# Kernel tuning notes

Hardware: AMD Instinct MI355X
Metric: run time of the kernel (lower is better)

Reference implementation:

```python
import jax, jax.numpy as jnp
import numpy as np

B, HI, WI, CV, CT, T = 8, 64, 64, 512, 512, 77
HH, DH = 8, 64
TOP_M, TOPP, CLAMP_LOGIT, TAU, ALPHA0 = 5, 0.9, 2.0, 0.5, 0.1


def setup_inputs() -> dict:
    key = jax.random.key(0)
    ks = jax.random.split(key, 12)
    s = 0.02
    w = lambda k, shp: jax.random.normal(k, shp, jnp.float32) * s
    return {
        "visual": jax.random.normal(ks[0], (B, HI, WI, CV), jnp.float32),
        "text": jax.random.normal(ks[1], (B, T, CT), jnp.float32),
        "ln1_g": jnp.ones((CV,), jnp.float32), "ln1_b": jnp.zeros((CV,), jnp.float32),
        "ln2_g": jnp.ones((CV,), jnp.float32), "ln2_b": jnp.zeros((CV,), jnp.float32),
        "Wq": w(ks[2], (CV, CV)), "bq": jnp.zeros((CV,), jnp.float32),
        "Wk": w(ks[3], (CT, CV)), "bk": jnp.zeros((CV,), jnp.float32),
        "Wv": w(ks[4], (CT, CV)), "bv": jnp.zeros((CV,), jnp.float32),
        "Wo": w(ks[5], (CV, CV)), "bo": jnp.zeros((CV,), jnp.float32),
        "Wg": w(ks[6], (CV, 1)), "bg": jnp.zeros((1,), jnp.float32),
        "W1": w(ks[7], (CV, 4 * CV)), "b1": jnp.zeros((4 * CV,), jnp.float32),
        "W2": w(ks[8], (4 * CV, CV)), "b2": jnp.zeros((CV,), jnp.float32),
        "logit_scale": jnp.asarray(np.log(1.0 / 0.07), jnp.float32),
        "alpha": jnp.asarray(ALPHA0, jnp.float32),
    }


def _ln(x, g, b, eps=1e-5):
    m = x.mean(-1, keepdims=True)
    v = ((x - m) ** 2).mean(-1, keepdims=True)
    return (x - m) * jax.lax.rsqrt(v + eps) * g + b


def _l2norm(t, eps=1e-6):  # F.normalize: x / max(||x||, eps)
    return t / jnp.maximum(jnp.linalg.norm(t, axis=-1, keepdims=True), eps)


def _sam_forward(visual, text, ln1_g, ln1_b, ln2_g, ln2_b, Wq, bq, Wk, bk, Wv, bv,
                 Wo, bo, Wg, bg, W1, b1, W2, b2, logit_scale, alpha):
    Bx, Hi, Wi, C = visual.shape
    N = Hi * Wi
    x = _ln(visual, ln1_g, ln1_b).reshape(Bx, N, C)          # pre-LN, [B,N,Cv]
    q_full = x @ Wq + bq
    k_full = text @ Wk + bk
    v_full = text @ Wv + bv
    pad = jnp.abs(text).sum(-1) <= 1e-6                      # [B,T] all-zero tokens
    q = _l2norm(q_full).reshape(Bx, N, HH, DH)               # normalize over full Cv, then split heads
    k = _l2norm(k_full).reshape(Bx, -1, HH, DH)
    v = v_full.reshape(Bx, -1, HH, DH)
    scale = jnp.exp(jnp.clip(logit_scale, -CLAMP_LOGIT, CLAMP_LOGIT)) / jnp.sqrt(jnp.float32(DH))
    sim = jnp.einsum("bnhd,bthd->bnht", q, k) * scale        # [B,N,H,T]
    sim = jnp.where(pad[:, None, None, :], -jnp.inf, sim)
    # top-m sparsify (keep entries >= kth largest)
    if TOP_M < sim.shape[-1]:
        kth = jax.lax.top_k(sim, TOP_M)[0][..., -1:]
        sim = jnp.where(sim >= kth, sim, -jnp.inf)
    attn = jax.nn.softmax(sim, axis=-1)
    # top-p nucleus: sort desc, keep cum<=p (always keep top-1), scatter back, renorm
    idx = jnp.argsort(-attn, axis=-1)
    prob = jnp.take_along_axis(attn, idx, axis=-1)
    keep = (jnp.cumsum(prob, axis=-1) <= TOPP).astype(attn.dtype)
    keep = keep.at[..., 0].set(1.0)
    inv = jnp.argsort(idx, axis=-1)
    sparse = jnp.take_along_axis(keep * prob, inv, axis=-1)
    attn = sparse / jnp.maximum(sparse.sum(-1, keepdims=True), 1e-6)
    # entropy-based confidence, [B,N,1]
    ah = attn.transpose(0, 2, 1, 3)                          # [B,H,N,T]
    maxp = ah.max(-1, keepdims=True)
    t_eff = jnp.maximum((ah > 0).astype(attn.dtype).sum(-1, keepdims=True), 1.0)
    denom = jnp.log(jnp.maximum(t_eff, 2.0))
    pc = jnp.maximum(ah, 1e-8)
    entropy = -(pc * jnp.log(pc)).sum(-1, keepdims=True) / denom
    conf = jnp.clip(maxp * (1.0 - entropy), 0.0, 1.0).mean(axis=1)
    aligned = jnp.einsum("bnht,bthd->bnhd", attn, v).reshape(Bx, N, C)
    aligned = aligned @ Wo + bo
    # trust region: cap ||aligned|| at tau * rms(x)
    x_rms = jnp.sqrt((x ** 2).mean(-1, keepdims=True)) + 1e-6
    a_norm = jnp.sqrt((aligned ** 2).sum(-1, keepdims=True))
    aligned = aligned * jnp.minimum(TAU * x_rms / jnp.maximum(a_norm, 1e-6), 1.0)
    gate = jax.nn.sigmoid(x @ Wg + bg) * conf
    y = x + alpha * gate * aligned
    h = jax.nn.gelu(_ln(y, ln2_g, ln2_b) @ W1 + b1, approximate=False)
    y = y + (h @ W2 + b2)
    return y.reshape(Bx, Hi, Wi, C)


def reference(visual, text, ln1_g, ln1_b, ln2_g, ln2_b, Wq, bq, Wk, bk, Wv, bv,
              Wo, bo, Wg, bg, W1, b1, W2, b2, logit_scale, alpha):
    return _sam_forward(visual, text, ln1_g, ln1_b, ln2_g, ln2_b, Wq, bq, Wk, bk,
                        Wv, bv, Wo, bo, Wg, bg, W1, b1, W2, b2, logit_scale, alpha)
```

## Files before the change

kernel.cpp:

```cpp
#include <hip/hip_runtime.h>
#include <hip/hip_bf16.h>
#include <math.h>

#define NROW 32768
#define CVC  512
#define T77  77
#define BT   616
#define HHC  8
#define DHC  64

typedef __attribute__((ext_vector_type(8))) short bf16x8;
typedef __attribute__((ext_vector_type(4))) float f32x4;

__device__ __forceinline__ void gload_lds16(const void* g, void* l) {
  __builtin_amdgcn_global_load_lds(
      (__attribute__((address_space(1))) void*)g,
      (__attribute__((address_space(3))) void*)l, 16, 0, 0);
}

__device__ __forceinline__ float wave_reduce_sum(float v) {
  #pragma unroll
  for (int s = 32; s > 0; s >>= 1) v += __shfl_xor(v, s, 64);
  return v;
}

__global__ __launch_bounds__(256)
void stats1_kernel(const float* __restrict__ visual, const float* __restrict__ g,
                   const float* __restrict__ b, const float* __restrict__ Wg,
                   const float* __restrict__ bg,
                   float* __restrict__ mean1, float* __restrict__ rstd1,
                   float* __restrict__ xrms, float* __restrict__ gpre,
                   __hip_bfloat16* __restrict__ xbf) {
  const int lane = threadIdx.x & 63;
  const int row  = blockIdx.x * 4 + (threadIdx.x >> 6);
  const float* vr = visual + (size_t)row * CVC + lane * 8;
  float4 va = *(const float4*)vr;
  float4 vb = *(const float4*)(vr + 4);
  float v[8] = {va.x, va.y, va.z, va.w, vb.x, vb.y, vb.z, vb.w};
  float s = 0.f;
  #pragma unroll
  for (int i = 0; i < 8; i++) s += v[i];
  float m = wave_reduce_sum(s) * (1.0f / CVC);
  float s2 = 0.f;
  #pragma unroll
  for (int i = 0; i < 8; i++) { float d = v[i] - m; s2 += d * d; }
  float rs = rsqrtf(wave_reduce_sum(s2) * (1.0f / CVC) + 1e-5f);
  const float4 g0 = *(const float4*)(g + lane * 8), g1v = *(const float4*)(g + lane * 8 + 4);
  const float4 b0 = *(const float4*)(b + lane * 8), b1v = *(const float4*)(b + lane * 8 + 4);
  const float4 w0 = *(const float4*)(Wg + lane * 8), w1 = *(const float4*)(Wg + lane * 8 + 4);
  float gg[8] = {g0.x, g0.y, g0.z, g0.w, g1v.x, g1v.y, g1v.z, g1v.w};
  float bb[8] = {b0.x, b0.y, b0.z, b0.w, b1v.x, b1v.y, b1v.z, b1v.w};
  float ww[8] = {w0.x, w0.y, w0.z, w0.w, w1.x, w1.y, w1.z, w1.w};
  float x[8], sx2 = 0.f, sg = 0.f;
  union { bf16x8 v8; __hip_bfloat16 h[8]; } u;
  #pragma unroll
  for (int i = 0; i < 8; i++) {
    x[i] = (v[i] - m) * rs * gg[i] + bb[i];
    sx2 += x[i] * x[i];
    sg  += x[i] * ww[i];
    u.h[i] = __float2bfloat16(x[i]);
  }
  *(bf16x8*)(xbf + (size_t)row * CVC + lane * 8) = u.v8;
  sx2 = wave_reduce_sum(sx2);
  sg  = wave_reduce_sum(sg);
  if (lane == 0) {
    mean1[row] = m; rstd1[row] = rs;
    xrms[row] = sqrtf(sx2 * (1.0f / CVC)) + 1e-6f;
    gpre[row] = sg + bg[0];
  }
}

__global__ void convT_kernel(const float* __restrict__ W, __hip_bfloat16* __restrict__ Wt,
                             int K, int N) {
  __shared__ float t[32][33];
  int n0 = blockIdx.x * 32, k0 = blockIdx.y * 32;
  int tx = threadIdx.x, ty = threadIdx.y;
  #pragma unroll
  for (int i = 0; i < 32; i += 8) t[ty + i][tx] = W[(size_t)(k0 + ty + i) * N + n0 + tx];
  __syncthreads();
  #pragma unroll
  for (int i = 0; i < 32; i += 8)
    Wt[(size_t)(n0 + ty + i) * K + k0 + tx] = __float2bfloat16(t[tx][ty + i]);
}

template<int EPI>
__global__ __launch_bounds__(512, 2)
void mfma_gemm(const __hip_bfloat16* __restrict__ A, const __hip_bfloat16* __restrict__ Bt,
               const float* __restrict__ bias, float* __restrict__ out,
               __hip_bfloat16* __restrict__ outbf, int M, int N, int K) {
  __shared__ __align__(16) char lds[131072];
  const int tid = threadIdx.x;
  const int lane = tid & 63;
  const int wid  = tid >> 6;

  const int nwg  = gridDim.x * gridDim.y;
  const int orig = blockIdx.y * gridDim.x + blockIdx.x;
  const int wg   = (orig & 7) * (nwg >> 3) + (orig >> 3);
  const int bx = wg % gridDim.x;
  const int by = wg / gridDim.x;
  const int bm = by * 256, bn = bx * 256;

  const int wm = wid >> 2, wn = wid & 3;
  const int lrow = lane & 15, kq = lane >> 4;

  f32x4 acc[8][4] = {};

  const int r_in = lane >> 3;
  const int cblk = (lane & 7) ^ r_in;
  const __hip_bfloat16* gA = A  + (size_t)(bm + r_in) * K + cblk * 8;
  const __hip_bfloat16* gB = Bt + (size_t)(bn + r_in) * K + cblk * 8;
  char* ldsA = lds;
  char* ldsB = lds + 65536;

  auto stageA = [&](int buf, int k0, int half) {
    #pragma unroll
    for (int j = 0; j < 2; j++) {
      int R0 = half * 128 + wid * 16 + j * 8;
      gload_lds16(gA + (size_t)R0 * K + k0, ldsA + buf * 32768 + R0 * 128);
    }
  };
  auto stageB = [&](int buf, int k0, int half) {
    #pragma unroll
    for (int j = 0; j < 2; j++) {
      int R0 = half * 128 + wid * 16 + j * 8;
      gload_lds16(gB + (size_t)R0 * K + k0, ldsB + buf * 32768 + R0 * 128);
    }
  };

  const int swz = lrow & 7;
  auto ldA = [&](int buf, int m, int kk) -> bf16x8 {
    int r = wm * 128 + m * 16 + lrow;
    int blk = (kk * 4 + kq) ^ swz;
    return *(const bf16x8*)(ldsA + buf * 32768 + r * 128 + blk * 16);
  };
  auto ldB = [&](int buf, int n, int kk) -> bf16x8 {
    int r = wn * 64 + n * 16 + lrow;
    int blk = (kk * 4 + kq) ^ swz;
    return *(const bf16x8*)(ldsB + buf * 32768 + r * 128 + blk * 16);
  };

  const int NT = K >> 6;
  stageB(0, 0, 0); stageB(0, 0, 1);
  stageA(0, 0, 0); stageA(0, 0, 1);
  stageB(1, 64, 0); stageB(1, 64, 1);

  bf16x8 af[4][2], bfv[4][2];
  for (int t = 0; t < NT; ++t) {
    const int cur = t & 1;
    if (t < NT - 1) {
      asm volatile("s_waitcnt vmcnt(4)" ::: "memory");
    } else {
      asm volatile("s_waitcnt vmcnt(0)" ::: "memory");
    }
    __builtin_amdgcn_s_barrier();
    asm volatile("" ::: "memory");

    #pragma unroll
    for (int m = 0; m < 4; m++) { af[m][0] = ldA(cur, m, 0); af[m][1] = ldA(cur, m, 1); }
    #pragma unroll
    for (int n = 0; n < 2; n++) { bfv[n][0] = ldB(cur, n, 0); bfv[n][1] = ldB(cur, n, 1); }
    if (t + 1 < NT) stageA(cur ^ 1, (t + 1) << 6, 0);
    __builtin_amdgcn_s_setprio(1);
    #pragma unroll
    for (int m = 0; m < 4; m++)
      #pragma unroll
      for (int n = 0; n < 2; n++) {
        acc[m][n] = __builtin_amdgcn_mfma_f32_16x16x32_bf16(af[m][0], bfv[n][0], acc[m][n], 0, 0, 0);
        acc[m][n] = __builtin_amdgcn_mfma_f32_16x16x32_bf16(af[m][1], bfv[n][1], acc[m][n], 0, 0, 0);
      }
    __builtin_amdgcn_s_setprio(0);

    #pragma unroll
    for (int n = 2; n < 4; n++) { bfv[n][0] = ldB(cur, n, 0); bfv[n][1] = ldB(cur, n, 1); }
    if (t + 1 < NT) stageA(cur ^ 1, (t + 1) << 6, 1);
    __builtin_amdgcn_s_setprio(1);
    #pragma unroll
    for (int m = 0; m < 4; m++)
      #pragma unroll
      for (int n = 2; n < 4; n++) {
        acc[m][n] = __builtin_amdgcn_mfma_f32_16x16x32_bf16(af[m][0], bfv[n][0], acc[m][n], 0, 0, 0);
        acc[m][n] = __builtin_amdgcn_mfma_f32_16x16x32_bf16(af[m][1], bfv[n][1], acc[m][n], 0, 0, 0);
      }
    __builtin_amdgcn_s_setprio(0);

    asm volatile("s_waitcnt lgkmcnt(0)" ::: "memory");
    __builtin_amdgcn_s_barrier();
    asm volatile("" ::: "memory");

    #pragma unroll
    for (int m = 0; m < 4; m++) { af[m][0] = ldA(cur, m + 4, 0); af[m][1] = ldA(cur, m + 4, 1); }
    if (t + 2 < NT) stageB(cur, (t + 2) << 6, 0);
    __builtin_amdgcn_s_setprio(1);
    #pragma unroll
    for (int m = 0; m < 4; m++)
      #pragma unroll
      for (int n = 0; n < 2; n++) {
        acc[m + 4][n] = __builtin_amdgcn_mfma_f32_16x16x32_bf16(af[m][0], bfv[n][0], acc[m + 4][n], 0, 0, 0);
        acc[m + 4][n] = __builtin_amdgcn_mfma_f32_16x16x32_bf16(af[m][1], bfv[n][1], acc[m + 4][n], 0, 0, 0);
      }
    __builtin_amdgcn_s_setprio(0);

    if (t + 2 < NT) stageB(cur, (t + 2) << 6, 1);
    __builtin_amdgcn_s_setprio(1);
    #pragma unroll
    for (int m = 0; m < 4; m++)
      #pragma unroll
      for (int n = 2; n < 4; n++) {
        acc[m + 4][n] = __builtin_amdgcn_mfma_f32_16x16x32_bf16(af[m][0], bfv[n][0], acc[m + 4][n], 0, 0, 0);
        acc[m + 4][n] = __builtin_amdgcn_mfma_f32_16x16x32_bf16(af[m][1], bfv[n][1], acc[m + 4][n], 0, 0, 0);
      }
    __builtin_amdgcn_s_setprio(0);
  }

  const int c0 = bn + wn * 64 + lrow;
  if (EPI == 1) {
    __syncthreads();
    char* eb = lds + wid * 16384;
    #pragma unroll
    for (int n = 0; n < 4; n++) {
      float bval = bias[c0 + n * 16];
      #pragma unroll
      for (int m = 0; m < 8; m++) {
        #pragma unroll
        for (int rg = 0; rg < 4; rg++) {
          int lr  = m * 16 + kq * 4 + rg;
          int lcb = (n * 32 + lrow * 2) ^ (kq << 5);
          float v = acc[m][n][rg] + bval;
          float ge = v / (1.0f + __expf(v * (-1.5957691216f - 0.0713548162f * v * v)));
          *(__hip_bfloat16*)(eb + lr * 128 + lcb) = __float2bfloat16(ge);
        }
      }
    }
    asm volatile("s_waitcnt lgkmcnt(0)" ::: "memory");
    __builtin_amdgcn_sched_barrier(0);
    const int rr = lane >> 3, bb = lane & 7;
    #pragma unroll
    for (int it = 0; it < 16; it++) {
      int lr  = it * 8 + rr;
      int lcb = (bb << 4) ^ (((lr >> 2) & 3) << 5);
      uint4 v = *(const uint4*)(eb + lr * 128 + lcb);
      size_t go = (size_t)(bm + wm * 128 + lr) * N + (bn + wn * 64 + bb * 8);
      *(uint4*)(&outbf[go]) = v;
    }
  } else {
    __syncthreads();
    char* eb = lds + wid * 16384;
    const int rr = lane >> 4, bb = lane & 15;
    #pragma unroll
    for (int half = 0; half < 2; half++) {
      if (half) {
        asm volatile("s_waitcnt lgkmcnt(0)" ::: "memory");
        __builtin_amdgcn_sched_barrier(0);
      }
      #pragma unroll
      for (int n = 0; n < 4; n++) {
        float bval = bias[c0 + n * 16];
        #pragma unroll
        for (int m = 0; m < 4; m++) {
          #pragma unroll
          for (int rg = 0; rg < 4; rg++) {
            int lr  = m * 16 + kq * 4 + rg;
            int byo = (n * 64 + lrow * 4) ^ (kq << 6);
            *(float*)(eb + lr * 256 + byo) = acc[half * 4 + m][n][rg] + bval;
          }
        }
      }
      asm volatile("s_waitcnt lgkmcnt(0)" ::: "memory");
      __builtin_amdgcn_sched_barrier(0);
      #pragma unroll
      for (int it = 0; it < 16; it++) {
        int lr  = it * 4 + rr;
        int byo = (bb * 16) ^ (((lr >> 2) & 3) << 6);
        float4 v4 = *(const float4*)(eb + lr * 256 + byo);
        size_t go = (size_t)(bm + wm * 128 + half * 64 + lr) * N + (bn + wn * 64 + bb * 4);
        if (EPI == 0) {
          *(float4*)(&out[go]) = v4;
        } else {
          const float4 o = *(const float4*)(&out[go]);
          v4.x += o.x; v4.y += o.y; v4.z += o.z; v4.w += o.w;
          *(float4*)(&out[go]) = v4;
        }
      }
    }
  }
}

__global__ void kv_gemm(const float* __restrict__ A, const float* __restrict__ W,
                        const float* __restrict__ bias, float* __restrict__ out,
                        int M, int K, int N) {
  __shared__ float As[16][68];
  __shared__ float Bs[16][68];
  int tid = threadIdx.x;
  int bm = blockIdx.y * 64, bn = blockIdx.x * 64;
  int ty = tid >> 4, tx = tid & 15;
  float acc[4][4] = {};
  for (int k0 = 0; k0 < K; k0 += 16) {
    #pragma unroll
    for (int i = 0; i < 4; i++) {
      int idx = tid + i * 256;
      int mm = idx >> 4, kk = idx & 15;
      int row = bm + mm;
      As[kk][mm] = (row < M) ? A[(size_t)row * K + k0 + kk] : 0.f;
    }
    #pragma unroll
    for (int i = 0; i < 4; i++) {
      int idx = tid + i * 256;
      int kk = idx >> 6, nn = idx & 63;
      Bs[kk][nn] = W[(size_t)(k0 + kk) * N + bn + nn];
    }
    __syncthreads();
    #pragma unroll
    for (int kk = 0; kk < 16; kk++) {
      float4 av = *(const float4*)&As[kk][ty * 4];
      float4 bv = *(const float4*)&Bs[kk][tx * 4];
      float a_[4] = {av.x, av.y, av.z, av.w};
      float b_[4] = {bv.x, bv.y, bv.z, bv.w};
      #pragma unroll
      for (int i = 0; i < 4; i++)
        #pragma unroll
        for (int j = 0; j < 4; j++)
          acc[i][j] = fmaf(a_[i], b_[j], acc[i][j]);
    }
    __syncthreads();
  }
  #pragma unroll
  for (int i = 0; i < 4; i++) {
    int row = bm + ty * 4 + i;
    if (row >= M) continue;
    #pragma unroll
    for (int j = 0; j < 4; j++) {
      int col = bn + tx * 4 + j;
      out[(size_t)row * N + col] = acc[i][j] + bias[col];
    }
  }
}

__global__ __launch_bounds__(256)
void l2norm_kernel(const float* __restrict__ buf, __hip_bfloat16* __restrict__ qbf) {
  const int lane = threadIdx.x & 63;
  const int row  = blockIdx.x * 4 + (threadIdx.x >> 6);
  const float* p = buf + (size_t)row * CVC + lane * 8;
  float4 va = *(const float4*)p;
  float4 vb = *(const float4*)(p + 4);
  float v[8] = {va.x, va.y, va.z, va.w, vb.x, vb.y, vb.z, vb.w};
  float s = 0.f;
  #pragma unroll
  for (int i = 0; i < 8; i++) s += v[i] * v[i];
  s = wave_reduce_sum(s);
  float inv = 1.0f / fmaxf(sqrtf(s), 1e-6f);
  union { bf16x8 v8; __hip_bfloat16 h[8]; } u;
  #pragma unroll
  for (int i = 0; i < 8; i++) u.h[i] = __float2bfloat16(v[i] * inv);
  *(bf16x8*)(qbf + (size_t)row * CVC + lane * 8) = u.v8;
}

__global__ __launch_bounds__(256)
void knorm_kernel(float* __restrict__ kf, const float* __restrict__ text,
                  int* __restrict__ pad) {
  const int lane = threadIdx.x & 63;
  const int row  = blockIdx.x * 4 + (threadIdx.x >> 6);
  float* p = kf + (size_t)row * CVC + lane * 8;
  const float* tx = text + (size_t)row * CVC + lane * 8;
  float4 va = *(const float4*)p;
  float4 vb = *(const float4*)(p + 4);
  float4 ta = *(const float4*)tx;
  float4 tb = *(const float4*)(tx + 4);
  float v[8] = {va.x, va.y, va.z, va.w, vb.x, vb.y, vb.z, vb.w};
  float t[8] = {ta.x, ta.y, ta.z, ta.w, tb.x, tb.y, tb.z, tb.w};
  float s = 0.f, a = 0.f;
  #pragma unroll
  for (int i = 0; i < 8; i++) { s += v[i] * v[i]; a += fabsf(t[i]); }
  s = wave_reduce_sum(s);
  a = wave_reduce_sum(a);
  float inv = 1.0f / fmaxf(sqrtf(s), 1e-6f);
  float4 o0 = {v[0] * inv, v[1] * inv, v[2] * inv, v[3] * inv};
  float4 o1 = {v[4] * inv, v[5] * inv, v[6] * inv, v[7] * inv};
  *(float4*)p = o0;
  *(float4*)(p + 4) = o1;
  if (lane == 0) pad[row] = (a <= 1e-6f) ? 1 : 0;
}

__global__ void kbf_kernel(const float* __restrict__ kf, __hip_bfloat16* __restrict__ kbf) {
  int bh = blockIdx.x;
  int b = bh >> 3, h = bh & 7;
  int tid = threadIdx.x;
  for (int i = tid; i < 80 * 64; i += 256) {
    int t = i >> 6, d = i & 63;
    float v = (t < T77) ? kf[(size_t)(b * T77 + t) * CVC + h * DHC + d] : 0.0f;
    kbf[(size_t)bh * (80 * 64) + i] = __float2bfloat16(v);
  }
}

__global__ __launch_bounds__(256)
void simA_kernel(const __hip_bfloat16* __restrict__ qbf, const __hip_bfloat16* __restrict__ kbf,
                 float* __restrict__ sim) {
  const int tid = threadIdx.x;
  const int wid = tid >> 6, lane = tid & 63;
  const int r0 = blockIdx.x * 64 + wid * 16;
  const int b = (blockIdx.x * 64) >> 12;
  const int lrow = lane & 15, kq = lane >> 4;
  const __hip_bfloat16* qrow = qbf + (size_t)(r0 + lrow) * CVC;
  for (int h = 0; h < HHC; h++) {
    const __hip_bfloat16* kb = kbf + (size_t)(b * 8 + h) * (80 * 64);
    f32x4 acc[5] = {};
    #pragma unroll
    for (int ks = 0; ks < 2; ks++) {
      bf16x8 af = *(const bf16x8*)(qrow + h * DHC + ks * 32 + kq * 8);
      #pragma unroll
      for (int n = 0; n < 5; n++) {
        bf16x8 bf = *(const bf16x8*)(kb + (size_t)(n * 16 + lrow) * DHC + ks * 32 + kq * 8);
        acc[n] = __builtin_amdgcn_mfma_f32_16x16x32_bf16(af, bf, acc[n], 0, 0, 0);
      }
    }
    #pragma unroll
    for (int n = 0; n < 5; n++)
      #pragma unroll
      for (int rg = 0; rg < 4; rg++)
        sim[(size_t)(r0 + kq * 4 + rg) * 640 + h * 80 + n * 16 + lrow] = acc[n][rg];
  }
}

__global__ __launch_bounds__(256)
void attnB_kernel(const float* __restrict__ sim, const float* __restrict__ vf,
                  const int* __restrict__ pad, const float* __restrict__ ls,
                  float* __restrict__ conf_out, __hip_bfloat16* __restrict__ abf) {
  __shared__ float spr[32][HHC][5];
  __shared__ int   sti[32][HHC][5];
  __shared__ float sconf[256];
  __shared__ float sbias[80];
  const int tid = threadIdx.x;
  const int r = tid >> 3, h = tid & 7;
  const int r0 = blockIdx.x * 32;
  const int b = r0 >> 12;
  const float lsv = fminf(fmaxf(ls[0], -2.0f), 2.0f);
  const float scale = expf(lsv) * 0.125f;

  if (tid < 80) sbias[tid] = (tid < T77 && !pad[b * T77 + tid]) ? 0.0f : -INFINITY;
  __syncthreads();

  float t0 = -INFINITY, t1 = -INFINITY, t2 = -INFINITY, t3 = -INFINITY, t4 = -INFINITY;
  int   i0 = -1, i1 = -1, i2 = -1, i3 = -1, i4 = -1;
  const float4* simp = (const float4*)(sim + (size_t)(r0 + r) * 640 + h * 80);
  #pragma unroll
  for (int tt = 0; tt < 20; tt++) {
    float4 v4 = simp[tt];
    #pragma unroll
    for (int j = 0; j < 4; j++) {
      int t = tt * 4 + j;
      float sv = (j == 0 ? v4.x : j == 1 ? v4.y : j == 2 ? v4.z : v4.w);
      float s = sv * scale + sbias[t];
      if (s > t4) {
        t4 = s; i4 = t;
        if (t4 > t3) { float f = t3; t3 = t4; t4 = f; int x = i3; i3 = i4; i4 = x; }
        if (t3 > t2) { float f = t2; t2 = t3; t3 = f; int x = i2; i2 = i3; i3 = x; }
        if (t2 > t1) { float f = t1; t1 = t2; t2 = f; int x = i1; i1 = i2; i2 = x; }
        if (t1 > t0) { float f = t0; t0 = t1; t1 = f; int x = i0; i0 = i1; i1 = x; }
      }
    }
  }

  float e0 = (t0 == -INFINITY) ? 0.f : expf(t0 - t0);
  float e1 = (t1 == -INFINITY) ? 0.f : expf(t1 - t0);
  float e2 = (t2 == -INFINITY) ? 0.f : expf(t2 - t0);
  float e3 = (t3 == -INFINITY) ? 0.f : expf(t3 - t0);
  float e4 = (t4 == -INFINITY) ? 0.f : expf(t4 - t0);
  float invs = 1.0f / (e0 + e1 + e2 + e3 + e4);
  float p0 = e0 * invs, p1 = e1 * invs, p2 = e2 * invs, p3 = e3 * invs, p4 = e4 * invs;
  float c1 = p0 + p1, c2 = c1 + p2, c3 = c2 + p3, c4 = c3 + p4;
  bool k1 = (c1 <= 0.9f), k2 = (c2 <= 0.9f), k3 = (c3 <= 0.9f), k4 = (c4 <= 0.9f);
  float skeep = p0 + (k1 ? p1 : 0.f) + (k2 ? p2 : 0.f) + (k3 ? p3 : 0.f) + (k4 ? p4 : 0.f);
  float rn = 1.0f / fmaxf(skeep, 1e-6f);
  float w0 = p0 * rn, w1 = k1 ? p1 * rn : 0.f, w2 = k2 ? p2 * rn : 0.f,
        w3 = k3 ? p3 * rn : 0.f, w4 = k4 ? p4 * rn : 0.f;
  int nnz = (w0 > 0.f) + (w1 > 0.f) + (w2 > 0.f) + (w3 > 0.f) + (w4 > 0.f);
  float ent = 0.f;
  {
    float pc;
    pc = fmaxf(w0, 1e-8f); ent -= pc * logf(pc);
    pc = fmaxf(w1, 1e-8f); ent -= pc * logf(pc);
    pc = fmaxf(w2, 1e-8f); ent -= pc * logf(pc);
    pc = fmaxf(w3, 1e-8f); ent -= pc * logf(pc);
    pc = fmaxf(w4, 1e-8f); ent -= pc * logf(pc);
  }
  ent += (float)(T77 - 5) * 1.8420681e-7f;
  float denom = logf(fmaxf(fmaxf((float)nnz, 1.0f), 2.0f));
  ent /= denom;
  float confh = fminf(fmaxf(w0 * (1.0f - ent), 0.f), 1.f);

  spr[r][h][0] = w0; spr[r][h][1] = w1; spr[r][h][2] = w2; spr[r][h][3] = w3; spr[r][h][4] = w4;
  sti[r][h][0] = i0; sti[r][h][1] = i1; sti[r][h][2] = i2; sti[r][h][3] = i3; sti[r][h][4] = i4;
  sconf[tid] = confh;
  __syncthreads();

  if (tid < 32) {
    float s = 0.f;
    #pragma unroll
    for (int j = 0; j < 8; j++) s += sconf[tid * 8 + j];
    conf_out[r0 + tid] = s * 0.125f;
  }

  #pragma unroll
  for (int it = 0; it < 64; it++) {
    int idx = tid + it * 256;
    int rr = idx >> 9, c = idx & 511, hh = c >> 6;
    float a = 0.f;
    #pragma unroll
    for (int i = 0; i < 5; i++) {
      float pr = spr[rr][hh][i]; int t = sti[rr][hh][i];
      if (pr > 0.f && t >= 0) a = fmaf(pr, vf[((size_t)(b * T77 + t)) * CVC + c], a);
    }
    abf[(size_t)(r0 + rr) * CVC + c] = __float2bfloat16(a);
  }
}

__global__ __launch_bounds__(256)
void combine_kernel(const float* __restrict__ al1, const float* __restrict__ visual,
                    const float* __restrict__ m1, const float* __restrict__ r1,
                    const float* __restrict__ g1, const float* __restrict__ b1v,
                    const float* __restrict__ xrms, const float* __restrict__ gpre,
                    const float* __restrict__ conf, const float* __restrict__ alpha,
                    const float* __restrict__ g2, const float* __restrict__ b2v,
                    float* __restrict__ dout, __hip_bfloat16* __restrict__ ybf) {
  const int lane = threadIdx.x & 63;
  const int row  = blockIdx.x * 4 + (threadIdx.x >> 6);
  const float* ar = al1 + (size_t)row * CVC + lane * 8;
  float4 aa = *(const float4*)ar;
  float4 ab = *(const float4*)(ar + 4);
  float av[8] = {aa.x, aa.y, aa.z, aa.w, ab.x, ab.y, ab.z, ab.w};
  float s2 = 0.f;
  #pragma unroll
  for (int i = 0; i < 8; i++) s2 += av[i] * av[i];
  s2 = wave_reduce_sum(s2);
  float an = sqrtf(s2);
  float factor = fminf(0.5f * xrms[row] / fmaxf(an, 1e-6f), 1.0f);
  float gate = conf[row] / (1.0f + expf(-gpre[row]));
  float coef = alpha[0] * gate * factor;
  float mm = m1[row], rs = r1[row];
  const float* vr = visual + (size_t)row * CVC + lane * 8;
  float4 va = *(const float4*)vr;
  float4 vb = *(const float4*)(vr + 4);
  float v[8] = {va.x, va.y, va.z, va.w, vb.x, vb.y, vb.z, vb.w};
  const float4 ga = *(const float4*)(g1 + lane * 8), gb = *(const float4*)(g1 + lane * 8 + 4);
  const float4 ba = *(const float4*)(b1v + lane * 8), bb2 = *(const float4*)(b1v + lane * 8 + 4);
  float gg[8] = {ga.x, ga.y, ga.z, ga.w, gb.x, gb.y, gb.z, gb.w};
  float bbv[8] = {ba.x, ba.y, ba.z, ba.w, bb2.x, bb2.y, bb2.z, bb2.w};
  float y[8], sy = 0.f;
  #pragma unroll
  for (int i = 0; i < 8; i++) {
    float x = (v[i] - mm) * rs * gg[i] + bbv[i];
    y[i] = x + coef * av[i];
    sy += y[i];
  }
  float* orow = dout + (size_t)row * CVC + lane * 8;
  float4 o0 = {y[0], y[1], y[2], y[3]};
  float4 o1 = {y[4], y[5], y[6], y[7]};
  *(float4*)orow = o0;
  *(float4*)(orow + 4) = o1;
  float ym = wave_reduce_sum(sy) * (1.0f / CVC);
  float var = 0.f;
  #pragma unroll
  for (int i = 0; i < 8; i++) { float d = y[i] - ym; var += d * d; }
  var = wave_reduce_sum(var) * (1.0f / CVC);
  float rs2 = rsqrtf(var + 1e-5f);
  const float4 g2a = *(const float4*)(g2 + lane * 8), g2b = *(const float4*)(g2 + lane * 8 + 4);
  const float4 b2a = *(const float4*)(b2v + lane * 8), b2b = *(const float4*)(b2v + lane * 8 + 4);
  float g2v[8] = {g2a.x, g2a.y, g2a.z, g2a.w, g2b.x, g2b.y, g2b.z, g2b.w};
  float b2vv[8] = {b2a.x, b2a.y, b2a.z, b2a.w, b2b.x, b2b.y, b2b.z, b2b.w};
  union { bf16x8 v8; __hip_bfloat16 h[8]; } u;
  #pragma unroll
  for (int i = 0; i < 8; i++)
    u.h[i] = __float2bfloat16((y[i] - ym) * rs2 * g2v[i] + b2vv[i]);
  *(bf16x8*)(ybf + (size_t)row * CVC + lane * 8) = u.v8;
}

extern "C" void kernel_launch(void* const* d_in, const int* in_sizes, int n_in,
                              void* d_out, int out_size, void* d_ws, size_t ws_size,
                              hipStream_t stream) {
  const float* visual = (const float*)d_in[0];
  const float* text   = (const float*)d_in[1];
  const float* ln1_g  = (const float*)d_in[2];
  const float* ln1_b  = (const float*)d_in[3];
  const float* ln2_g  = (const float*)d_in[4];
  const float* ln2_b  = (const float*)d_in[5];
  const float* Wq = (const float*)d_in[6];  const float* bq = (const float*)d_in[7];
  const float* Wk = (const float*)d_in[8];  const float* bk = (const float*)d_in[9];
  const float* Wv = (const float*)d_in[10]; const float* bv = (const float*)d_in[11];
  const float* Wo = (const float*)d_in[12]; const float* bo = (const float*)d_in[13];
  const float* Wg = (const float*)d_in[14]; const float* bg = (const float*)d_in[15];
  const float* W1 = (const float*)d_in[16]; const float* b1 = (const float*)d_in[17];
  const float* W2 = (const float*)d_in[18]; const float* b2 = (const float*)d_in[19];
  const float* ls    = (const float*)d_in[20];
  const float* alpha = (const float*)d_in[21];
  float* out = (float*)d_out;

  char* base = (char*)d_ws;
  __hip_bfloat16* H   = (__hip_bfloat16*)base;
  float* BUFA = (float*)base;
  float* SIM  = (float*)base;
  float* BUFB = (float*)(base + ((size_t)64 << 20));
  __hip_bfloat16* CBF = (__hip_bfloat16*)(base + ((size_t)128 << 20));
  char* p = base + ((size_t)160 << 20);
  __hip_bfloat16* WqT = (__hip_bfloat16*)p; p += (size_t)512 * 512 * 2;
  __hip_bfloat16* WoT = (__hip_bfloat16*)p; p += (size_t)512 * 512 * 2;
  __hip_bfloat16* W1T = (__hip_bfloat16*)p; p += (size_t)2048 * 512 * 2;
  __hip_bfloat16* W2T = (__hip_bfloat16*)p; p += (size_t)512 * 2048 * 2;
  float* KF = (float*)p; p += (size_t)BT * CVC * 4;
  float* VF = (float*)p; p += (size_t)BT * CVC * 4;
  int* PADF = (int*)p;  p += 4096;
  float* MEAN1 = (float*)p; p += (size_t)NROW * 4;
  float* RSTD1 = (float*)p; p += (size_t)NROW * 4;
  float* XRMS  = (float*)p; p += (size_t)NROW * 4;
  float* GPRE  = (float*)p; p += (size_t)NROW * 4;
  float* CONF  = (float*)p; p += (size_t)NROW * 4;
  __hip_bfloat16* KBF = (__hip_bfloat16*)p; p += (size_t)64 * 80 * 64 * 2;

  stats1_kernel<<<NROW / 4, 256, 0, stream>>>(visual, ln1_g, ln1_b, Wg, bg,
                                              MEAN1, RSTD1, XRMS, GPRE, CBF);
  convT_kernel<<<dim3(16, 16), dim3(32, 8), 0, stream>>>(Wq, WqT, 512, 512);
  convT_kernel<<<dim3(16, 16), dim3(32, 8), 0, stream>>>(Wo, WoT, 512, 512);
  convT_kernel<<<dim3(64, 16), dim3(32, 8), 0, stream>>>(W1, W1T, 512, 2048);
  convT_kernel<<<dim3(16, 64), dim3(32, 8), 0, stream>>>(W2, W2T, 2048, 512);

  mfma_gemm<0><<<dim3(2, 128), 512, 0, stream>>>(CBF, WqT, bq, BUFA, nullptr, NROW, 512, 512);
  l2norm_kernel<<<NROW / 4, 256, 0, stream>>>(BUFA, CBF);

  kv_gemm<<<dim3(8, 10), 256, 0, stream>>>(text, Wk, bk, KF, BT, CVC, CVC);
  kv_gemm<<<dim3(8, 10), 256, 0, stream>>>(text, Wv, bv, VF, BT, CVC, CVC);
  knorm_kernel<<<BT / 4, 256, 0, stream>>>(KF, text, PADF);
  kbf_kernel<<<64, 256, 0, stream>>>(KF, KBF);

  simA_kernel<<<NROW / 64, 256, 0, stream>>>(CBF, KBF, SIM);
  attnB_kernel<<<NROW / 32, 256, 0, stream>>>(SIM, VF, PADF, ls, CONF, CBF);

  mfma_gemm<0><<<dim3(2, 128), 512, 0, stream>>>(CBF, WoT, bo, BUFB, nullptr, NROW, 512, 512);

  combine_kernel<<<NROW / 4, 256, 0, stream>>>(BUFB, visual, MEAN1, RSTD1, ln1_g, ln1_b,
                                               XRMS, GPRE, CONF, alpha, ln2_g, ln2_b, out, CBF);

  mfma_gemm<1><<<dim3(8, 128), 512, 0, stream>>>(CBF, W1T, b1, nullptr, H, NROW, 2048, 512);

  mfma_gemm<2><<<dim3(2, 128), 512, 0, stream>>>(H, W2T, b2, out, nullptr, NROW, 512, 2048);
}
```

Baseline: 585.0 us.

## Fuse similarity MFMA and top-k attention into one kernel via LDS

The similarity kernel and the top-k/softmax/aggregate kernel are merged into one kernel. Per-head similarity tiles are staged in shared memory, four heads at a time, instead of a 640-wide fp32 similarity matrix being written to global memory and read back. This removes a large global round trip and one launch. In exchange each block processes 64 rows and uses a lot of LDS, which limits occupancy. The K and V projection GEMMs are also combined into a single launch that picks its weights by block index.

```diff
diff --git a/kernel.cpp b/kernel.cpp
--- a/kernel.cpp
+++ b/kernel.cpp
@@ -285,13 +285,19 @@
   }
 }
 
-__global__ void kv_gemm(const float* __restrict__ A, const float* __restrict__ W,
-                        const float* __restrict__ bias, float* __restrict__ out,
-                        int M, int K, int N) {
+__global__ void kv2_gemm(const float* __restrict__ A,
+                         const float* __restrict__ Wk, const float* __restrict__ bk,
+                         const float* __restrict__ Wv, const float* __restrict__ bv,
+                         float* __restrict__ KF, float* __restrict__ VF,
+                         int M, int K, int N) {
   __shared__ float As[16][68];
   __shared__ float Bs[16][68];
+  const bool isV = blockIdx.y >= 10;
+  const float* W    = isV ? Wv : Wk;
+  const float* bias = isV ? bv : bk;
+  float* out        = isV ? VF : KF;
   int tid = threadIdx.x;
-  int bm = blockIdx.y * 64, bn = blockIdx.x * 64;
+  int bm = (isV ? blockIdx.y - 10 : blockIdx.y) * 64, bn = blockIdx.x * 64;
   int ty = tid >> 4, tx = tid & 15;
   float acc[4][4] = {};
   for (int k0 = 0; k0 < K; k0 += 16) {
@@ -312,9 +318,9 @@
     #pragma unroll
     for (int kk = 0; kk < 16; kk++) {
       float4 av = *(const float4*)&As[kk][ty * 4];
-      float4 bv = *(const float4*)&Bs[kk][tx * 4];
+      float4 bv4 = *(const float4*)&Bs[kk][tx * 4];
       float a_[4] = {av.x, av.y, av.z, av.w};
-      float b_[4] = {bv.x, bv.y, bv.z, bv.w};
+      float b_[4] = {bv4.x, bv4.y, bv4.z, bv4.w};
       #pragma unroll
       for (int i = 0; i < 4; i++)
         #pragma unroll
@@ -392,115 +398,116 @@
 }
 
 __global__ __launch_bounds__(256)
-void simA_kernel(const __hip_bfloat16* __restrict__ qbf, const __hip_bfloat16* __restrict__ kbf,
-                 float* __restrict__ sim) {
+void attn_fused(const __hip_bfloat16* __restrict__ qbf, const __hip_bfloat16* __restrict__ kbf,
+                const float* __restrict__ vf, const int* __restrict__ pad,
+                const float* __restrict__ ls, float* __restrict__ conf_out,
+                __hip_bfloat16* __restrict__ abf) {
+  __shared__ __align__(16) float simLDS[4][64][84];
+  __shared__ float spr[64][HHC][5];
+  __shared__ int   sti[64][HHC][5];
+  __shared__ float sconf[HHC][64];
+  __shared__ float sbias[80];
   const int tid = threadIdx.x;
   const int wid = tid >> 6, lane = tid & 63;
-  const int r0 = blockIdx.x * 64 + wid * 16;
-  const int b = (blockIdx.x * 64) >> 12;
+  const int r0 = blockIdx.x * 64;
+  const int b  = r0 >> 12;
   const int lrow = lane & 15, kq = lane >> 4;
-  const __hip_bfloat16* qrow = qbf + (size_t)(r0 + lrow) * CVC;
-  for (int h = 0; h < HHC; h++) {
-    const __hip_bfloat16* kb = kbf + (size_t)(b * 8 + h) * (80 * 64);
-    f32x4 acc[5] = {};
-    #pragma unroll
-    for (int ks = 0; ks < 2; ks++) {
-      bf16x8 af = *(const bf16x8*)(qrow + h * DHC + ks * 32 + kq * 8);
-      #pragma unroll
-      for (int n = 0; n < 5; n++) {
-        bf16x8 bf = *(const bf16x8*)(kb + (size_t)(n * 16 + lrow) * DHC + ks * 32 + kq * 8);
-        acc[n] = __builtin_amdgcn_mfma_f32_16x16x32_bf16(af, bf, acc[n], 0, 0, 0);
-      }
-    }
-    #pragma unroll
-    for (int n = 0; n < 5; n++)
-      #pragma unroll
-      for (int rg = 0; rg < 4; rg++)
-        sim[(size_t)(r0 + kq * 4 + rg) * 640 + h * 80 + n * 16 + lrow] = acc[n][rg];
-  }
-}
-
-__global__ __launch_bounds__(256)
-void attnB_kernel(const float* __restrict__ sim, const float* __restrict__ vf,
-                  const int* __restrict__ pad, const float* __restrict__ ls,
-                  float* __restrict__ conf_out, __hip_bfloat16* __restrict__ abf) {
-  __shared__ float spr[32][HHC][5];
-  __shared__ int   sti[32][HHC][5];
-  __shared__ float sconf[256];
-  __shared__ float sbias[80];
-  const int tid = threadIdx.x;
-  const int r = tid >> 3, h = tid & 7;
-  const int r0 = blockIdx.x * 32;
-  const int b = r0 >> 12;
   const float lsv = fminf(fmaxf(ls[0], -2.0f), 2.0f);
   const float scale = expf(lsv) * 0.125f;
 
   if (tid < 80) sbias[tid] = (tid < T77 && !pad[b * T77 + tid]) ? 0.0f : -INFINITY;
+
+  const __hip_bfloat16* qrow = qbf + (size_t)(r0 + wid * 16 + lrow) * CVC;
+
+  for (int hg = 0; hg < 2; hg++) {
+    if (hg) __syncthreads();
+    #pragma unroll
+    for (int h4 = 0; h4 < 4; h4++) {
+      int h = hg * 4 + h4;
+      const __hip_bfloat16* kb = kbf + (size_t)(b * 8 + h) * (80 * 64);
+      f32x4 acc[5] = {};
+      #pragma unroll
+      for (int ks = 0; ks < 2; ks++) {
+        bf16x8 af = *(const bf16x8*)(qrow + h * DHC + ks * 32 + kq * 8);
+        #pragma unroll
+        for (int n = 0; n < 5; n++) {
+          bf16x8 bf = *(const bf16x8*)(kb + (size_t)(n * 16 + lrow) * DHC + ks * 32 + kq * 8);
+          acc[n] = __builtin_amdgcn_mfma_f32_16x16x32_bf16(af, bf, acc[n], 0, 0, 0);
+        }
+      }
+      #pragma unroll
+      for (int n = 0; n < 5; n++)
+        #pragma unroll
+        for (int rg = 0; rg < 4; rg++)
+          simLDS[h4][wid * 16 + kq * 4 + rg][n * 16 + lrow] = acc[n][rg];
+    }
+    __syncthreads();
+
+    {
+      const int hh = wid, r = lane;
+      const int h = hg * 4 + hh;
+      float t0 = -INFINITY, t1 = -INFINITY, t2 = -INFINITY, t3 = -INFINITY, t4 = -INFINITY;
+      int   i0 = -1, i1 = -1, i2 = -1, i3 = -1, i4 = -1;
+      const float4* simp = (const float4*)&simLDS[hh][r][0];
+      #pragma unroll
+      for (int tt = 0; tt < 20; tt++) {
+        float4 v4 = simp[tt];
+        #pragma unroll
+        for (int j = 0; j < 4; j++) {
+          int t = tt * 4 + j;
+          float sv = (j == 0 ? v4.x : j == 1 ? v4.y : j == 2 ? v4.z : v4.w);
+          float s = sv * scale + sbias[t];
+          if (s > t4) {
+            t4 = s; i4 = t;
+            if (t4 > t3) { float f = t3; t3 = t4; t4 = f; int x = i3; i3 = i4; i4 = x; }
+            if (t3 > t2) { float f = t2; t2 = t3; t3 = f; int x = i2; i2 = i3; i3 = x; }
+            if (t2 > t1) { float f = t1; t1 = t2; t2 = f; int x = i1; i1 = i2; i2 = x; }
+            if (t1 > t0) { float f = t0; t0 = t1; t1 = f; int x = i0; i0 = i1; i1 = x; }
+          }
+        }
+      }
+      float e0 = (t0 == -INFINITY) ? 0.f : expf(t0 - t0);
+      float e1 = (t1 == -INFINITY) ? 0.f : expf(t1 - t0);
+      float e2 = (t2 == -INFINITY) ? 0.f : expf(t2 - t0);
+      float e3 = (t3 == -INFINITY) ? 0.f : expf(t3 - t0);
+      float e4 = (t4 == -INFINITY) ? 0.f : expf(t4 - t0);
+      float invs = 1.0f / (e0 + e1 + e2 + e3 + e4);
+      float p0 = e0 * invs, p1 = e1 * invs, p2 = e2 * invs, p3 = e3 * invs, p4 = e4 * invs;
+      float c1 = p0 + p1, c2 = c1 + p2, c3 = c2 + p3, c4 = c3 + p4;
+      bool k1 = (c1 <= 0.9f), k2 = (c2 <= 0.9f), k3 = (c3 <= 0.9f), k4 = (c4 <= 0.9f);
+      float skeep = p0 + (k1 ? p1 : 0.f) + (k2 ? p2 : 0.f) + (k3 ? p3 : 0.f) + (k4 ? p4 : 0.f);
+      float rn = 1.0f / fmaxf(skeep, 1e-6f);
+      float w0 = p0 * rn, w1 = k1 ? p1 * rn : 0.f, w2 = k2 ? p2 * rn : 0.f,
+            w3 = k3 ? p3 * rn : 0.f, w4 = k4 ? p4 * rn : 0.f;
+      int nnz = (w0 > 0.f) + (w1 > 0.f) + (w2 > 0.f) + (w3 > 0.f) + (w4 > 0.f);
+      float ent = 0.f;
+      {
+        float pc;
+        pc = fmaxf(w0, 1e-8f); ent -= pc * logf(pc);
+        pc = fmaxf(w1, 1e-8f); ent -= pc * logf(pc);
+        pc = fmaxf(w2, 1e-8f); ent -= pc * logf(pc);
+        pc = fmaxf(w3, 1e-8f); ent -= pc * logf(pc);
+        pc = fmaxf(w4, 1e-8f); ent -= pc * logf(pc);
+      }
+      ent += (float)(T77 - 5) * 1.8420681e-7f;
+      float denom = logf(fmaxf(fmaxf((float)nnz, 1.0f), 2.0f));
+      ent /= denom;
+      float confh = fminf(fmaxf(w0 * (1.0f - ent), 0.f), 1.f);
+      spr[r][h][0] = w0; spr[r][h][1] = w1; spr[r][h][2] = w2; spr[r][h][3] = w3; spr[r][h][4] = w4;
+      sti[r][h][0] = i0; sti[r][h][1] = i1; sti[r][h][2] = i2; sti[r][h][3] = i3; sti[r][h][4] = i4;
+      sconf[h][r] = confh;
+    }
+  }
   __syncthreads();
 
-  float t0 = -INFINITY, t1 = -INFINITY, t2 = -INFINITY, t3 = -INFINITY, t4 = -INFINITY;
-  int   i0 = -1, i1 = -1, i2 = -1, i3 = -1, i4 = -1;
-  const float4* simp = (const float4*)(sim + (size_t)(r0 + r) * 640 + h * 80);
-  #pragma unroll
-  for (int tt = 0; tt < 20; tt++) {
-    float4 v4 = simp[tt];
-    #pragma unroll
-    for (int j = 0; j < 4; j++) {
-      int t = tt * 4 + j;
-      float sv = (j == 0 ? v4.x : j == 1 ? v4.y : j == 2 ? v4.z : v4.w);
-      float s = sv * scale + sbias[t];
-      if (s > t4) {
-        t4 = s; i4 = t;
-        if (t4 > t3) { float f = t3; t3 = t4; t4 = f; int x = i3; i3 = i4; i4 = x; }
-        if (t3 > t2) { float f = t2; t2 = t3; t3 = f; int x = i2; i2 = i3; i3 = x; }
-        if (t2 > t1) { float f = t1; t1 = t2; t2 = f; int x = i1; i1 = i2; i2 = x; }
-        if (t1 > t0) { float f = t0; t0 = t1; t1 = f; int x = i0; i0 = i1; i1 = x; }
-      }
-    }
-  }
-
-  float e0 = (t0 == -INFINITY) ? 0.f : expf(t0 - t0);
-  float e1 = (t1 == -INFINITY) ? 0.f : expf(t1 - t0);
-  float e2 = (t2 == -INFINITY) ? 0.f : expf(t2 - t0);
-  float e3 = (t3 == -INFINITY) ? 0.f : expf(t3 - t0);
-  float e4 = (t4 == -INFINITY) ? 0.f : expf(t4 - t0);
-  float invs = 1.0f / (e0 + e1 + e2 + e3 + e4);
-  float p0 = e0 * invs, p1 = e1 * invs, p2 = e2 * invs, p3 = e3 * invs, p4 = e4 * invs;
-  float c1 = p0 + p1, c2 = c1 + p2, c3 = c2 + p3, c4 = c3 + p4;
-  bool k1 = (c1 <= 0.9f), k2 = (c2 <= 0.9f), k3 = (c3 <= 0.9f), k4 = (c4 <= 0.9f);
-  float skeep = p0 + (k1 ? p1 : 0.f) + (k2 ? p2 : 0.f) + (k3 ? p3 : 0.f) + (k4 ? p4 : 0.f);
-  float rn = 1.0f / fmaxf(skeep, 1e-6f);
-  float w0 = p0 * rn, w1 = k1 ? p1 * rn : 0.f, w2 = k2 ? p2 * rn : 0.f,
-        w3 = k3 ? p3 * rn : 0.f, w4 = k4 ? p4 * rn : 0.f;
-  int nnz = (w0 > 0.f) + (w1 > 0.f) + (w2 > 0.f) + (w3 > 0.f) + (w4 > 0.f);
-  float ent = 0.f;
-  {
-    float pc;
-    pc = fmaxf(w0, 1e-8f); ent -= pc * logf(pc);
-    pc = fmaxf(w1, 1e-8f); ent -= pc * logf(pc);
-    pc = fmaxf(w2, 1e-8f); ent -= pc * logf(pc);
-    pc = fmaxf(w3, 1e-8f); ent -= pc * logf(pc);
-    pc = fmaxf(w4, 1e-8f); ent -= pc * logf(pc);
-  }
-  ent += (float)(T77 - 5) * 1.8420681e-7f;
-  float denom = logf(fmaxf(fmaxf((float)nnz, 1.0f), 2.0f));
-  ent /= denom;
-  float confh = fminf(fmaxf(w0 * (1.0f - ent), 0.f), 1.f);
-
-  spr[r][h][0] = w0; spr[r][h][1] = w1; spr[r][h][2] = w2; spr[r][h][3] = w3; spr[r][h][4] = w4;
-  sti[r][h][0] = i0; sti[r][h][1] = i1; sti[r][h][2] = i2; sti[r][h][3] = i3; sti[r][h][4] = i4;
-  sconf[tid] = confh;
-  __syncthreads();
-
-  if (tid < 32) {
+  if (tid < 64) {
     float s = 0.f;
     #pragma unroll
-    for (int j = 0; j < 8; j++) s += sconf[tid * 8 + j];
+    for (int j = 0; j < 8; j++) s += sconf[j][tid];
     conf_out[r0 + tid] = s * 0.125f;
   }
 
-  #pragma unroll
-  for (int it = 0; it < 64; it++) {
+  for (int it = 0; it < 128; it++) {
     int idx = tid + it * 256;
     int rr = idx >> 9, c = idx & 511, hh = c >> 6;
     float a = 0.f;
@@ -596,7 +603,6 @@
   char* base = (char*)d_ws;
   __hip_bfloat16* H   = (__hip_bfloat16*)base;
   float* BUFA = (float*)base;
-  float* SIM  = (float*)base;
   float* BUFB = (float*)(base + ((size_t)64 << 20));
   __hip_bfloat16* CBF = (__hip_bfloat16*)(base + ((size_t)128 << 20));
   char* p = base + ((size_t)160 << 20);
@@ -624,13 +630,11 @@
   mfma_gemm<0><<<dim3(2, 128), 512, 0, stream>>>(CBF, WqT, bq, BUFA, nullptr, NROW, 512, 512);
   l2norm_kernel<<<NROW / 4, 256, 0, stream>>>(BUFA, CBF);
 
-  kv_gemm<<<dim3(8, 10), 256, 0, stream>>>(text, Wk, bk, KF, BT, CVC, CVC);
-  kv_gemm<<<dim3(8, 10), 256, 0, stream>>>(text, Wv, bv, VF, BT, CVC, CVC);
+  kv2_gemm<<<dim3(8, 20), 256, 0, stream>>>(text, Wk, bk, Wv, bv, KF, VF, BT, CVC, CVC);
   knorm_kernel<<<BT / 4, 256, 0, stream>>>(KF, text, PADF);
   kbf_kernel<<<64, 256, 0, stream>>>(KF, KBF);
 
-  simA_kernel<<<NROW / 64, 256, 0, stream>>>(CBF, KBF, SIM);
-  attnB_kernel<<<NROW / 32, 256, 0, stream>>>(SIM, VF, PADF, ls, CONF, CBF);
+  attn_fused<<<NROW / 64, 256, 0, stream>>>(CBF, KBF, VF, PADF, ls, CONF, CBF);
 
   mfma_gemm<0><<<dim3(2, 128), 512, 0, stream>>>(CBF, WoT, bo, BUFB, nullptr, NROW, 512, 512);
 
```

Result: slower. 653.3 us (+11.7%).
